# Performance work log

Measured on AMD Instinct MI355X. Metric: run time of the kernel, lower is better.

## Reference

```python
import jax, jax.numpy as jnp
import numpy as np

N_NODES = 100000
N_EDGES = 1600000
N_GRAPHS = 512
IN_CH = 128
HID = 128
OUT_CH = 1
FP_DIM = 2048


def prelu(x, a):
    return jnp.where(x > 0, x, a * x)


def setup_inputs() -> dict:
    key = jax.random.key(0)
    ks = jax.random.split(key, 16)

    def glorot(k, shape):
        lim = np.sqrt(6.0 / (shape[0] + shape[1]))
        return jax.random.uniform(k, shape, jnp.float32, -lim, lim)

    x = jax.random.normal(ks[0], (N_NODES, IN_CH), jnp.float32)
    fp = jax.random.normal(ks[1], (N_GRAPHS, FP_DIM), jnp.float32)
    edge_index = jax.random.randint(ks[2], (2, N_EDGES), 0, N_NODES, jnp.int64)
    batch = jnp.sort(jax.random.randint(ks[3], (N_NODES,), 0, N_GRAPHS, jnp.int64))

    params = {
        "W_pre": glorot(ks[4], (IN_CH, HID)),
        "b_pre": jnp.zeros((HID,), jnp.float32),
        "a_pre": jnp.full((HID,), 0.25, jnp.float32),
        "Wl1": glorot(ks[5], (HID, HID)),
        "bl1": jnp.zeros((HID,), jnp.float32),
        "Wr1": glorot(ks[6], (HID, HID)),
        "a1": jnp.full((HID,), 0.25, jnp.float32),
        "Wl2": glorot(ks[7], (HID, HID)),
        "bl2": jnp.zeros((HID,), jnp.float32),
        "Wr2": glorot(ks[8], (HID, HID)),
        "a2": jnp.full((HID,), 0.25, jnp.float32),
        "W_fp": glorot(ks[9], (FP_DIM, HID)),
        "b_fp": jnp.zeros((HID,), jnp.float32),
        "a_fp": jnp.full((HID,), 0.25, jnp.float32),
        "W_post": glorot(ks[10], (2 * HID, OUT_CH)),
        "b_post": jnp.zeros((OUT_CH,), jnp.float32),
    }
    return dict(x=x, fp=fp, edge_index=edge_index, batch=batch, **params)


def sage_conv(x, src, dst, Wl, bl, Wr):
    # aggr='sum': sum messages x[src] into dst, then lin_l(agg)+bias + lin_r(x)
    agg = jax.ops.segment_sum(x[src], dst, num_segments=N_NODES)  # [N, H]
    return agg @ Wl + bl + x @ Wr


def reference(x, fp, edge_index, batch,
              W_pre, b_pre, a_pre,
              Wl1, bl1, Wr1, a1,
              Wl2, bl2, Wr2, a2,
              W_fp, b_fp, a_fp,
              W_post, b_post):
    src, dst = edge_index[0], edge_index[1]
    # pre_mp (dropout is identity at eval)
    h = prelu(x @ W_pre + b_pre, a_pre)
    # message passing
    h = prelu(sage_conv(h, src, dst, Wl1, bl1, Wr1), a1)
    h = prelu(sage_conv(h, src, dst, Wl2, bl2, Wr2), a2)
    # global mean pool over graphs
    sums = jax.ops.segment_sum(h, batch, num_segments=N_GRAPHS)  # [G, H]
    counts = jax.ops.segment_sum(jnp.ones((h.shape[0],), h.dtype), batch,
                                 num_segments=N_GRAPHS)
    pooled = sums / jnp.maximum(counts, 1.0)[:, None]
    # fingerprint head
    fp_emb = prelu(fp @ W_fp + b_fp, a_fp)
    # post mp
    out = jnp.concatenate([pooled, fp_emb], axis=1) @ W_post + b_post
    return out
```

## Files before the change

kernel.cpp:

```cpp
#include <hip/hip_runtime.h>

#define NN 100000
#define NE 1600000
#define NG 512
#define HID 128
#define FPD 2048
#define BSHIFT 8
#define NBUK ((NN + 255) >> 8)
#define BCAP 5120
#define EPB 4096
#define EPT 16

typedef _Float16 f16;
typedef __attribute__((ext_vector_type(8))) _Float16 f16x8;
typedef __attribute__((ext_vector_type(2))) _Float16 f16x2;
typedef __attribute__((ext_vector_type(4))) float f32x4;


__global__ __launch_bounds__(256) void bucket_scatter(const int* __restrict__ src,
                                                      const int* __restrict__ dst,
                                                      int* __restrict__ bcnt,
                                                      uint* __restrict__ bbuf, int E) {
  __shared__ int hist[NBUK];
  __shared__ int gbase[NBUK];
  __shared__ int lbase[NBUK + 1];
  __shared__ int sc[2][512];
  __shared__ uint stage[EPB];
  int t = threadIdx.x;
  int e0 = blockIdx.x * EPB;
  for (int i = t; i < NBUK; i += 256) hist[i] = 0;
  __syncthreads();

  int myb[EPT], myoff[EPT];
  uint myp[EPT];
#pragma unroll
  for (int u = 0; u < EPT; ++u) {
    int e = e0 + u * 256 + t;
    myb[u] = -1;
    if (e < E) {
      int d = dst[e];
      int b = d >> BSHIFT;
      myp[u] = ((uint)(d & 255) << 24) | (uint)src[e];
      myb[u] = b;
      myoff[u] = atomicAdd(&hist[b], 1);
    }
  }
  __syncthreads();

  sc[0][t] = (t < NBUK) ? hist[t] : 0;
  sc[0][t + 256] = (t + 256 < NBUK) ? hist[t + 256] : 0;
  int pp = 0;
  for (int off = 1; off < 512; off <<= 1) {
    __syncthreads();
    int a0 = sc[pp][t] + ((t >= off) ? sc[pp][t - off] : 0);
    int a1 = sc[pp][t + 256] + ((t + 256 >= off) ? sc[pp][t + 256 - off] : 0);
    sc[1 - pp][t] = a0;
    sc[1 - pp][t + 256] = a1;
    pp = 1 - pp;
  }
  __syncthreads();
  if (t < NBUK) lbase[t] = (t == 0) ? 0 : sc[pp][t - 1];
  if (t + 256 < NBUK) lbase[t + 256] = sc[pp][t + 255];
  if (t == 0) lbase[NBUK] = sc[pp][NBUK - 1];
  for (int i = t; i < NBUK; i += 256)
    if (hist[i] > 0) gbase[i] = atomicAdd(&bcnt[i], hist[i]);
  __syncthreads();

#pragma unroll
  for (int u = 0; u < EPT; ++u)
    if (myb[u] >= 0) stage[lbase[myb[u]] + myoff[u]] = myp[u];
  __syncthreads();

  int total = lbase[NBUK];
  for (int j = t; j < total; j += 256) {
    int lo = 0, hi = NBUK - 1;
    while (lo < hi) {
      int mid = (lo + hi + 1) >> 1;
      if (lbase[mid] <= j) lo = mid; else hi = mid - 1;
    }
    bbuf[(size_t)lo * BCAP + gbase[lo] + (j - lbase[lo])] = stage[j];
  }
}

__global__ __launch_bounds__(512) void scan_bcnt(const int* __restrict__ bcnt,
                                                 int* __restrict__ bbase,
                                                 int* __restrict__ rowptr) {
  __shared__ int lds[512];
  int t = threadIdx.x;
  int v = (t < NBUK) ? bcnt[t] : 0;
  lds[t] = v;
  __syncthreads();
  for (int off = 1; off < 512; off <<= 1) {
    int add = (t >= off) ? lds[t - off] : 0;
    __syncthreads();
    lds[t] += add;
    __syncthreads();
  }
  if (t < NBUK) bbase[t] = lds[t] - v;
  if (t == 0) {
    bbase[NBUK] = lds[511];
    rowptr[NN] = lds[511];
  }
}

__global__ __launch_bounds__(256) void bucket_finish(const int* __restrict__ bcnt,
                                                     const uint* __restrict__ bbuf,
                                                     const int* __restrict__ bbase,
                                                     int* __restrict__ rowptr,
                                                     int* __restrict__ cols) {
  __shared__ uint ebuf[BCAP];
  __shared__ int h[256];
  __shared__ int s2[256];
  __shared__ int cur[256];
  int b = blockIdx.x, t = threadIdx.x;
  h[t] = 0;
  __syncthreads();
  int n = bcnt[b];
  const uint* bb = bbuf + (size_t)b * BCAP;
  for (int e = t; e < n; e += 256) {
    uint w = bb[e];
    ebuf[e] = w;
    atomicAdd(&h[w >> 24], 1);
  }
  __syncthreads();
  int v = h[t];
  s2[t] = v;
  __syncthreads();
  for (int off = 1; off < 256; off <<= 1) {
    int add = (t >= off) ? s2[t - off] : 0;
    __syncthreads();
    s2[t] += add;
    __syncthreads();
  }
  int base = bbase[b] + s2[t] - v;
  int node = (b << BSHIFT) + t;
  if (node < NN) rowptr[node] = base;
  cur[t] = base;
  __syncthreads();
  for (int e = t; e < n; e += 256) {
    uint w = ebuf[e];
    int pos = atomicAdd(&cur[w >> 24], 1);
    cols[pos] = (int)(w & 0xFFFFFF);
  }
}


__global__ __launch_bounds__(256) void cvt_all(const float* __restrict__ w0,
                                               const float* __restrict__ w1,
                                               const float* __restrict__ w2,
                                               const float* __restrict__ w3,
                                               const float* __restrict__ w4,
                                               const float* __restrict__ Wfp,
                                               const float* __restrict__ fp,
                                               f16* __restrict__ Wt,
                                               f16* __restrict__ Wfpt,
                                               f16* __restrict__ fpb) {
  int idx = blockIdx.x * 256 + threadIdx.x;
  if (idx < 81920) {
    int w = idx >> 14, rem = idx & 16383;
    int j = rem >> 7, k = rem & 127;
    const float* W = (w == 0) ? w0 : (w == 1) ? w1 : (w == 2) ? w2 : (w == 3) ? w3 : w4;
    Wt[idx] = (f16)W[k * 128 + j];
  } else if (idx < 344064) {
    int id = idx - 81920;
    int j = id >> 11, k = id & 2047;
    Wfpt[id] = (f16)Wfp[k * 128 + j];
  } else if (idx < 606208) {
    int id = idx - 344064;
    float4 v = *reinterpret_cast<const float4*>(&fp[id * 4]);
    union { uint2 u; f16 h[4]; } o;
    o.h[0] = (f16)v.x; o.h[1] = (f16)v.y; o.h[2] = (f16)v.z; o.h[3] = (f16)v.w;
    *reinterpret_cast<uint2*>(&fpb[id * 4]) = o.u;
  }
}


__global__ __launch_bounds__(256) void agg_f16(const f16* __restrict__ H,
                                               const int* __restrict__ rowptr,
                                               const int* __restrict__ cols,
                                               f16* __restrict__ out) {
  int node = blockIdx.x * 4 + (threadIdx.x >> 6);
  int lane = threadIdx.x & 63;
  int q = lane >> 4;
  int sub = lane & 15;
  int s = rowptr[node], e = rowptr[node + 1];
  float acc[8] = {0.f, 0.f, 0.f, 0.f, 0.f, 0.f, 0.f, 0.f};
  union U { uint4 u; f16x2 h2[4]; f16 h[8]; };

  int i = s;
  for (; i + 15 < e; i += 16) {
    int c0 = cols[i + q];
    int c1 = cols[i + 4 + q];
    int c2 = cols[i + 8 + q];
    int c3 = cols[i + 12 + q];
    U v0, v1, v2, v3;
    v0.u = *reinterpret_cast<const uint4*>(&H[(size_t)c0 * 128 + sub * 8]);
    v1.u = *reinterpret_cast<const uint4*>(&H[(size_t)c1 * 128 + sub * 8]);
    v2.u = *reinterpret_cast<const uint4*>(&H[(size_t)c2 * 128 + sub * 8]);
    v3.u = *reinterpret_cast<const uint4*>(&H[(size_t)c3 * 128 + sub * 8]);
#pragma unroll
    for (int p = 0; p < 4; ++p) {
      f16x2 t01 = v0.h2[p] + v1.h2[p];
      f16x2 t23 = v2.h2[p] + v3.h2[p];
      f16x2 tt = t01 + t23;
      acc[2 * p]     += (float)tt[0];
      acc[2 * p + 1] += (float)tt[1];
    }
  }
  for (; i < e; i += 4) {
    int rem = e - i;
    if (q < rem) {
      U v;
      v.u = *reinterpret_cast<const uint4*>(&H[(size_t)cols[i + q] * 128 + sub * 8]);
#pragma unroll
      for (int z = 0; z < 8; ++z) acc[z] += (float)v.h[z];
    }
  }

#pragma unroll
  for (int z = 0; z < 8; ++z) {
    acc[z] += __shfl_xor(acc[z], 16);
    acc[z] += __shfl_xor(acc[z], 32);
  }
  if (q == 0) {
    union { uint4 u; f16 h[8]; } pk;
#pragma unroll
    for (int z = 0; z < 8; ++z) pk.h[z] = (f16)acc[z];
    *reinterpret_cast<uint4*>(&out[(size_t)node * 128 + sub * 8]) = pk.u;
  }
}


__global__ __launch_bounds__(256) void gemm_pre(const float* __restrict__ X,
                                                const f16* __restrict__ Wt,
                                                const float* __restrict__ bias,
                                                const float* __restrict__ pa,
                                                f16* __restrict__ out, int rows) {
  int t = threadIdx.x;
  int wave = t >> 6, lane = t & 63;
  int lrow = lane & 15, lk = lane >> 4;
  int r0 = blockIdx.x * 64;
  int n0 = wave << 1;

  const f16x8* Wv = reinterpret_cast<const f16x8*>(Wt);
  f16x8 w[2][4];
#pragma unroll
  for (int ni = 0; ni < 2; ++ni)
#pragma unroll
    for (int ks = 0; ks < 4; ++ks)
      w[ni][ks] = Wv[((((n0 + ni) << 4) + lrow) << 4) + (ks << 2) + lk];

  float bv[2], av[2];
#pragma unroll
  for (int ni = 0; ni < 2; ++ni) {
    int col = ((n0 + ni) << 4) + lrow;
    bv[ni] = bias[col];
    av[ni] = pa[col];
  }

#pragma unroll 2
  for (int rg = 0; rg < 4; ++rg) {
    int r = r0 + (rg << 4) + lrow;
    if (r > rows - 1) r = rows - 1;
    const float* xp = X + (size_t)r * 128 + (lk << 3);
    f16x8 a[4];
#pragma unroll
    for (int ks = 0; ks < 4; ++ks) {
      float4 v0 = *reinterpret_cast<const float4*>(xp + (ks << 5));
      float4 v1 = *reinterpret_cast<const float4*>(xp + (ks << 5) + 4);
      f16x8 av8;
      av8[0] = (f16)v0.x; av8[1] = (f16)v0.y; av8[2] = (f16)v0.z; av8[3] = (f16)v0.w;
      av8[4] = (f16)v1.x; av8[5] = (f16)v1.y; av8[6] = (f16)v1.z; av8[7] = (f16)v1.w;
      a[ks] = av8;
    }
    f32x4 acc[2] = {(f32x4){0.f, 0.f, 0.f, 0.f}, (f32x4){0.f, 0.f, 0.f, 0.f}};
#pragma unroll
    for (int ks = 0; ks < 4; ++ks)
#pragma unroll
      for (int ni = 0; ni < 2; ++ni)
        acc[ni] = __builtin_amdgcn_mfma_f32_16x16x32_f16(a[ks], w[ni][ks], acc[ni], 0, 0, 0);
#pragma unroll
    for (int ni = 0; ni < 2; ++ni) {
      int col = ((n0 + ni) << 4) + lrow;
#pragma unroll
      for (int j = 0; j < 4; ++j) {
        int rr = r0 + (rg << 4) + (lk << 2) + j;
        if (rr < rows) {
          float xv = acc[ni][j] + bv[ni];
          xv = xv > 0.f ? xv : av[ni] * xv;
          out[(size_t)rr * 128 + col] = (f16)xv;
        }
      }
    }
  }
}


__global__ __launch_bounds__(256) void gemm_f16(const f16* __restrict__ A1,
                                                const f16* __restrict__ A2,
                                                const f16* __restrict__ W1t,
                                                const f16* __restrict__ W2t,
                                                const float* __restrict__ bias,
                                                const float* __restrict__ pa,
                                                f16* __restrict__ Ch, int rows) {
  int t = threadIdx.x;
  int wave = t >> 6, lane = t & 63;
  int lrow = lane & 15, lk = lane >> 4;
  int r0 = blockIdx.x * 64;
  int n0 = wave << 1;

  const f16x8* Wv1 = reinterpret_cast<const f16x8*>(W1t);
  const f16x8* Wv2 = reinterpret_cast<const f16x8*>(W2t);

  f16x8 w1[2][4], w2[2][4];
#pragma unroll
  for (int ni = 0; ni < 2; ++ni)
#pragma unroll
    for (int ks = 0; ks < 4; ++ks) {
      int wi = ((((n0 + ni) << 4) + lrow) << 4) + (ks << 2) + lk;
      w1[ni][ks] = Wv1[wi];
      w2[ni][ks] = Wv2[wi];
    }

  float bv[2], av[2];
#pragma unroll
  for (int ni = 0; ni < 2; ++ni) {
    int col = ((n0 + ni) << 4) + lrow;
    bv[ni] = bias[col];
    av[ni] = pa[col];
  }

  f16x8 aA[2][4], aB[2][4];
  {
    int r = r0 + lrow;
    if (r > rows - 1) r = rows - 1;
    size_t off = (size_t)r * 128 + (lk << 3);
#pragma unroll
    for (int ks = 0; ks < 4; ++ks) {
      aA[0][ks] = *reinterpret_cast<const f16x8*>(A1 + off + (ks << 5));
      aB[0][ks] = *reinterpret_cast<const f16x8*>(A2 + off + (ks << 5));
    }
  }

#pragma unroll
  for (int rg = 0; rg < 4; ++rg) {
    int cur = rg & 1, nxt = cur ^ 1;
    if (rg < 3) {
      int rn = r0 + ((rg + 1) << 4) + lrow;
      if (rn > rows - 1) rn = rows - 1;
      size_t offn = (size_t)rn * 128 + (lk << 3);
#pragma unroll
      for (int ks = 0; ks < 4; ++ks) {
        aA[nxt][ks] = *reinterpret_cast<const f16x8*>(A1 + offn + (ks << 5));
        aB[nxt][ks] = *reinterpret_cast<const f16x8*>(A2 + offn + (ks << 5));
      }
    }
    f32x4 acc1[2] = {(f32x4){0.f, 0.f, 0.f, 0.f}, (f32x4){0.f, 0.f, 0.f, 0.f}};
    f32x4 acc2[2] = {(f32x4){0.f, 0.f, 0.f, 0.f}, (f32x4){0.f, 0.f, 0.f, 0.f}};
#pragma unroll
    for (int ks = 0; ks < 4; ++ks) {
#pragma unroll
      for (int ni = 0; ni < 2; ++ni) {
        acc1[ni] = __builtin_amdgcn_mfma_f32_16x16x32_f16(aA[cur][ks], w1[ni][ks], acc1[ni], 0, 0, 0);
        acc2[ni] = __builtin_amdgcn_mfma_f32_16x16x32_f16(aB[cur][ks], w2[ni][ks], acc2[ni], 0, 0, 0);
      }
    }
#pragma unroll
    for (int ni = 0; ni < 2; ++ni) {
      int col = ((n0 + ni) << 4) + lrow;
#pragma unroll
      for (int j = 0; j < 4; ++j) {
        int rr = r0 + (rg << 4) + (lk << 2) + j;
        if (rr < rows) {
          float xv = acc1[ni][j] + acc2[ni][j] + bv[ni];
          xv = xv > 0.f ? xv : av[ni] * xv;
          Ch[(size_t)rr * 128 + col] = (f16)xv;
        }
      }
    }
  }
}


__global__ __launch_bounds__(256) void fp_gemm(const f16* __restrict__ A,
                                               const f16* __restrict__ Wt,
                                               float* __restrict__ part) {
  int kc = blockIdx.x;
  int rb = blockIdx.y;
  int t = threadIdx.x;
  int wave = t >> 6, lane = t & 63;
  int lrow = lane & 15, lk = lane >> 4;
  int r0 = rb * 128;
  int n0 = wave << 1;

  const f16x8* Wv = reinterpret_cast<const f16x8*>(Wt);
  const f16x8* Av = reinterpret_cast<const f16x8*>(A);

  f16x8 w[2][4];
#pragma unroll
  for (int ni = 0; ni < 2; ++ni)
#pragma unroll
    for (int ks = 0; ks < 4; ++ks) {
      int j = ((n0 + ni) << 4) + lrow;
      w[ni][ks] = Wv[j * 256 + (kc << 4) + (ks << 2) + lk];
    }

#pragma unroll 2
  for (int rg = 0; rg < 8; ++rg) {
    int r = r0 + (rg << 4) + lrow;
    f16x8 a[4];
#pragma unroll
    for (int ks = 0; ks < 4; ++ks)
      a[ks] = Av[r * 256 + (kc << 4) + (ks << 2) + lk];
    f32x4 acc[2] = {(f32x4){0.f, 0.f, 0.f, 0.f}, (f32x4){0.f, 0.f, 0.f, 0.f}};
#pragma unroll
    for (int ks = 0; ks < 4; ++ks)
#pragma unroll
      for (int ni = 0; ni < 2; ++ni)
        acc[ni] = __builtin_amdgcn_mfma_f32_16x16x32_f16(a[ks], w[ni][ks], acc[ni], 0, 0, 0);
#pragma unroll
    for (int ni = 0; ni < 2; ++ni) {
      int col = ((n0 + ni) << 4) + lrow;
#pragma unroll
      for (int j = 0; j < 4; ++j) {
        int rr = r0 + (rg << 4) + (lk << 2) + j;
        part[((size_t)kc * 512 + rr) * 128 + col] = acc[ni][j];
      }
    }
  }
}


__device__ __forceinline__ int lower_bound_dev(const int* __restrict__ arr, int n, int val) {
  int lo = 0, hi = n;
  while (lo < hi) {
    int mid = (lo + hi) >> 1;
    if (arr[mid] < val) lo = mid + 1; else hi = mid;
  }
  return lo;
}

__global__ __launch_bounds__(512) void pool_final(const f16* __restrict__ H,
                                                  const int* __restrict__ batch,
                                                  const float* __restrict__ part,
                                                  const float* __restrict__ bfp,
                                                  const float* __restrict__ afp,
                                                  const float* __restrict__ Wp,
                                                  const float* __restrict__ bp,
                                                  float* __restrict__ out) {
  __shared__ float red[512];
  __shared__ float pf[256];
  int g = blockIdx.x;
  int t = threadIdx.x;
  int col = t & 127, rq = t >> 7;
  int start = lower_bound_dev(batch, NN, g);
  int end = lower_bound_dev(batch, NN, g + 1);
  float acc = 0.f;
  for (int r = start + rq; r < end; r += 4) acc += (float)H[(size_t)r * 128 + col];
  red[t] = acc;
  __syncthreads();
  if (t < 128) {
    float s = red[t] + red[128 + t] + red[256 + t] + red[384 + t];
    int c = end - start;
    pf[t] = s / (float)(c > 0 ? c : 1);
  } else if (t < 256) {
    int j = t - 128;
    float s = bfp[j];
#pragma unroll
    for (int kc = 0; kc < 16; ++kc) s += part[((size_t)kc * 512 + g) * 128 + j];
    float a = afp[j];
    pf[t] = s > 0.f ? s : a * s;
  }
  __syncthreads();
  if (t < 128) {
    float v = pf[t] * Wp[t] + pf[128 + t] * Wp[128 + t];
    red[t] = v;
  }
  __syncthreads();
  if (t < 64) {
    float v = red[t] + red[t + 64];
    for (int off = 32; off > 0; off >>= 1) v += __shfl_down(v, off);
    if (t == 0) out[g] = v + bp[0];
  }
}


extern "C" void kernel_launch(void* const* d_in, const int* in_sizes, int n_in,
                              void* d_out, int out_size, void* d_ws, size_t ws_size,
                              hipStream_t stream) {
  const float* x      = (const float*)d_in[0];
  const float* fp     = (const float*)d_in[1];
  const int*   ei     = (const int*)d_in[2];
  const int*   batch  = (const int*)d_in[3];
  const float* W_pre  = (const float*)d_in[4];
  const float* b_pre  = (const float*)d_in[5];
  const float* a_pre  = (const float*)d_in[6];
  const float* Wl1    = (const float*)d_in[7];
  const float* bl1    = (const float*)d_in[8];
  const float* Wr1    = (const float*)d_in[9];
  const float* a1     = (const float*)d_in[10];
  const float* Wl2    = (const float*)d_in[11];
  const float* bl2    = (const float*)d_in[12];
  const float* Wr2    = (const float*)d_in[13];
  const float* a2     = (const float*)d_in[14];
  const float* W_fp   = (const float*)d_in[15];
  const float* b_fp   = (const float*)d_in[16];
  const float* a_fp   = (const float*)d_in[17];
  const float* W_post = (const float*)d_in[18];
  const float* b_post = (const float*)d_in[19];

  const int* src = ei;
  const int* dst = ei + NE;

  const size_t NBUF = (size_t)NN * 128;
  f16* bufA = (f16*)d_ws;
  f16* bufB = bufA + NBUF;
  f16* bufC = bufB + NBUF;
  f16* Wt   = bufC + NBUF;
  f16* fpb  = Wt + 5 * 16384;
  f16* Wfpt = fpb + 512 * 2048;
  float* part = (float*)(Wfpt + 128 * 2048);
  int* rowptr  = (int*)(part + 16 * 512 * 128);
  int* bbase   = rowptr + NN + 4;
  int* bcnt    = bbase + NBUK + 4;
  int* colsA   = bcnt + ((NBUK + 3) & ~3);
  uint* bbuf   = (uint*)(colsA + NE);

  hipMemsetAsync(bcnt, 0, NBUK * sizeof(int), stream);
  bucket_scatter<<<(NE + EPB - 1) / EPB, 256, 0, stream>>>(src, dst, bcnt, bbuf, NE);
  scan_bcnt<<<1, 512, 0, stream>>>(bcnt, bbase, rowptr);
  bucket_finish<<<NBUK, 256, 0, stream>>>(bcnt, bbuf, bbase, rowptr, colsA);

  cvt_all<<<(606208 + 255) / 256, 256, 0, stream>>>(W_pre, Wl1, Wr1, Wl2, Wr2, W_fp, fp,
                                                    Wt, Wfpt, fpb);
  {
    dim3 g(16, 4);
    fp_gemm<<<g, 256, 0, stream>>>(fpb, Wfpt, part);
  }

  const f16* Wt_pre = Wt;
  const f16* Wt_l1  = Wt + 16384;
  const f16* Wt_r1  = Wt + 32768;
  const f16* Wt_l2  = Wt + 49152;
  const f16* Wt_r2  = Wt + 65536;

  int gGemm = (NN + 63) / 64;

  gemm_pre<<<gGemm, 256, 0, stream>>>(x, Wt_pre, b_pre, a_pre, bufA, NN);

  agg_f16<<<NN / 4, 256, 0, stream>>>(bufA, rowptr, colsA, bufC);
  gemm_f16<<<gGemm, 256, 0, stream>>>(bufC, bufA, Wt_l1, Wt_r1, bl1, a1, bufB, NN);

  agg_f16<<<NN / 4, 256, 0, stream>>>(bufB, rowptr, colsA, bufC);
  gemm_f16<<<gGemm, 256, 0, stream>>>(bufC, bufB, Wt_l2, Wt_r2, bl2, a2, bufA, NN);

  pool_final<<<NG, 512, 0, stream>>>(bufA, batch, part, b_fp, a_fp, W_post, b_post,
                                     (float*)d_out);
}
```

Baseline: 330.3 us.

## Pad CSR rows to multiples of 16 with dummy node and fuse fp conversion into fp_gemm

Each node's neighbour list is padded to a multiple of 16 entries that point at an all-zero dummy row (node NN), stored as separate start and end arrays. The aggregation kernel can then drop its remainder loop and always use the 4-wide unrolled gather. The fp-to-f16 conversion moves out of cvt_all and into fp_gemm, which reads fp32 directly, removing a write and read of an intermediate buffer. In exchange, padding adds extra gathered rows of the zero vector and two small memsets, and colsA needs a larger allocation.

```diff
diff --git a/kernel.cpp b/kernel.cpp
--- a/kernel.cpp
+++ b/kernel.cpp
@@ -10,6 +10,7 @@
 #define BCAP 5120
 #define EPB 4096
 #define EPT 16
+#define COLSCAP (NE + NBUK * 4096 + 64)
 
 typedef _Float16 f16;
 typedef __attribute__((ext_vector_type(8))) _Float16 f16x8;
@@ -83,11 +84,10 @@
 }
 
 __global__ __launch_bounds__(512) void scan_bcnt(const int* __restrict__ bcnt,
-                                                 int* __restrict__ bbase,
-                                                 int* __restrict__ rowptr) {
+                                                 int* __restrict__ bbase) {
   __shared__ int lds[512];
   int t = threadIdx.x;
-  int v = (t < NBUK) ? bcnt[t] : 0;
+  int v = (t < NBUK) ? (bcnt[t] + 4096) : 0;
   lds[t] = v;
   __syncthreads();
   for (int off = 1; off < 512; off <<= 1) {
@@ -97,16 +97,13 @@
     __syncthreads();
   }
   if (t < NBUK) bbase[t] = lds[t] - v;
-  if (t == 0) {
-    bbase[NBUK] = lds[511];
-    rowptr[NN] = lds[511];
-  }
 }
 
 __global__ __launch_bounds__(256) void bucket_finish(const int* __restrict__ bcnt,
                                                      const uint* __restrict__ bbuf,
                                                      const int* __restrict__ bbase,
-                                                     int* __restrict__ rowptr,
+                                                     int* __restrict__ astart,
+                                                     int* __restrict__ aend,
                                                      int* __restrict__ cols) {
   __shared__ uint ebuf[BCAP];
   __shared__ int h[256];
@@ -124,7 +121,8 @@
   }
   __syncthreads();
   int v = h[t];
-  s2[t] = v;
+  int pv = (v + 15) & ~15;
+  s2[t] = pv;
   __syncthreads();
   for (int off = 1; off < 256; off <<= 1) {
     int add = (t >= off) ? s2[t - off] : 0;
@@ -132,9 +130,12 @@
     s2[t] += add;
     __syncthreads();
   }
-  int base = bbase[b] + s2[t] - v;
+  int base = bbase[b] + s2[t] - pv;
   int node = (b << BSHIFT) + t;
-  if (node < NN) rowptr[node] = base;
+  if (node < NN) {
+    astart[node] = base;
+    aend[node] = base + pv;
+  }
   cur[t] = base;
   __syncthreads();
   for (int e = t; e < n; e += 256) {
@@ -142,6 +143,7 @@
     int pos = atomicAdd(&cur[w >> 24], 1);
     cols[pos] = (int)(w & 0xFFFFFF);
   }
+  for (int p = v; p < pv; ++p) cols[base + p] = NN;
 }
 
 
@@ -151,10 +153,8 @@
                                                const float* __restrict__ w3,
                                                const float* __restrict__ w4,
                                                const float* __restrict__ Wfp,
-                                               const float* __restrict__ fp,
                                                f16* __restrict__ Wt,
-                                               f16* __restrict__ Wfpt,
-                                               f16* __restrict__ fpb) {
+                                               f16* __restrict__ Wfpt) {
   int idx = blockIdx.x * 256 + threadIdx.x;
   if (idx < 81920) {
     int w = idx >> 14, rem = idx & 16383;
@@ -165,30 +165,24 @@
     int id = idx - 81920;
     int j = id >> 11, k = id & 2047;
     Wfpt[id] = (f16)Wfp[k * 128 + j];
-  } else if (idx < 606208) {
-    int id = idx - 344064;
-    float4 v = *reinterpret_cast<const float4*>(&fp[id * 4]);
-    union { uint2 u; f16 h[4]; } o;
-    o.h[0] = (f16)v.x; o.h[1] = (f16)v.y; o.h[2] = (f16)v.z; o.h[3] = (f16)v.w;
-    *reinterpret_cast<uint2*>(&fpb[id * 4]) = o.u;
   }
 }
 
 
 __global__ __launch_bounds__(256) void agg_f16(const f16* __restrict__ H,
-                                               const int* __restrict__ rowptr,
+                                               const int* __restrict__ astart,
+                                               const int* __restrict__ aend,
                                                const int* __restrict__ cols,
                                                f16* __restrict__ out) {
   int node = blockIdx.x * 4 + (threadIdx.x >> 6);
   int lane = threadIdx.x & 63;
   int q = lane >> 4;
   int sub = lane & 15;
-  int s = rowptr[node], e = rowptr[node + 1];
+  int s = astart[node], e = aend[node];
   float acc[8] = {0.f, 0.f, 0.f, 0.f, 0.f, 0.f, 0.f, 0.f};
   union U { uint4 u; f16x2 h2[4]; f16 h[8]; };
 
-  int i = s;
-  for (; i + 15 < e; i += 16) {
+  for (int i = s; i < e; i += 16) {
     int c0 = cols[i + q];
     int c1 = cols[i + 4 + q];
     int c2 = cols[i + 8 + q];
@@ -205,15 +199,6 @@
       f16x2 tt = t01 + t23;
       acc[2 * p]     += (float)tt[0];
       acc[2 * p + 1] += (float)tt[1];
-    }
-  }
-  for (; i < e; i += 4) {
-    int rem = e - i;
-    if (q < rem) {
-      U v;
-      v.u = *reinterpret_cast<const uint4*>(&H[(size_t)cols[i + q] * 128 + sub * 8]);
-#pragma unroll
-      for (int z = 0; z < 8; ++z) acc[z] += (float)v.h[z];
     }
   }
 
@@ -382,7 +367,7 @@
 }
 
 
-__global__ __launch_bounds__(256) void fp_gemm(const f16* __restrict__ A,
+__global__ __launch_bounds__(256) void fp_gemm(const float* __restrict__ FP,
                                                const f16* __restrict__ Wt,
                                                float* __restrict__ part) {
   int kc = blockIdx.x;
@@ -394,7 +379,6 @@
   int n0 = wave << 1;
 
   const f16x8* Wv = reinterpret_cast<const f16x8*>(Wt);
-  const f16x8* Av = reinterpret_cast<const f16x8*>(A);
 
   f16x8 w[2][4];
 #pragma unroll
@@ -408,10 +392,17 @@
 #pragma unroll 2
   for (int rg = 0; rg < 8; ++rg) {
     int r = r0 + (rg << 4) + lrow;
+    const float* xp = FP + (size_t)r * 2048 + (kc << 7) + (lk << 3);
     f16x8 a[4];
 #pragma unroll
-    for (int ks = 0; ks < 4; ++ks)
-      a[ks] = Av[r * 256 + (kc << 4) + (ks << 2) + lk];
+    for (int ks = 0; ks < 4; ++ks) {
+      float4 v0 = *reinterpret_cast<const float4*>(xp + (ks << 5));
+      float4 v1 = *reinterpret_cast<const float4*>(xp + (ks << 5) + 4);
+      f16x8 av8;
+      av8[0] = (f16)v0.x; av8[1] = (f16)v0.y; av8[2] = (f16)v0.z; av8[3] = (f16)v0.w;
+      av8[4] = (f16)v1.x; av8[5] = (f16)v1.y; av8[6] = (f16)v1.z; av8[7] = (f16)v1.w;
+      a[ks] = av8;
+    }
     f32x4 acc[2] = {(f32x4){0.f, 0.f, 0.f, 0.f}, (f32x4){0.f, 0.f, 0.f, 0.f}};
 #pragma unroll
     for (int ks = 0; ks < 4; ++ks)
@@ -512,30 +503,32 @@
   const int* src = ei;
   const int* dst = ei + NE;
 
-  const size_t NBUF = (size_t)NN * 128;
+  const size_t NBUF = (size_t)(NN + 1) * 128;
   f16* bufA = (f16*)d_ws;
   f16* bufB = bufA + NBUF;
   f16* bufC = bufB + NBUF;
   f16* Wt   = bufC + NBUF;
-  f16* fpb  = Wt + 5 * 16384;
-  f16* Wfpt = fpb + 512 * 2048;
+  f16* Wfpt = Wt + 5 * 16384;
   float* part = (float*)(Wfpt + 128 * 2048);
-  int* rowptr  = (int*)(part + 16 * 512 * 128);
-  int* bbase   = rowptr + NN + 4;
+  int* astart  = (int*)(part + 16 * 512 * 128);
+  int* aend    = astart + NN;
+  int* bbase   = aend + NN;
   int* bcnt    = bbase + NBUK + 4;
   int* colsA   = bcnt + ((NBUK + 3) & ~3);
-  uint* bbuf   = (uint*)(colsA + NE);
+  uint* bbuf   = (uint*)(colsA + COLSCAP);
 
   hipMemsetAsync(bcnt, 0, NBUK * sizeof(int), stream);
+  hipMemsetAsync(bufA + (size_t)NN * 128, 0, 256, stream);
+  hipMemsetAsync(bufB + (size_t)NN * 128, 0, 256, stream);
   bucket_scatter<<<(NE + EPB - 1) / EPB, 256, 0, stream>>>(src, dst, bcnt, bbuf, NE);
-  scan_bcnt<<<1, 512, 0, stream>>>(bcnt, bbase, rowptr);
-  bucket_finish<<<NBUK, 256, 0, stream>>>(bcnt, bbuf, bbase, rowptr, colsA);
-
-  cvt_all<<<(606208 + 255) / 256, 256, 0, stream>>>(W_pre, Wl1, Wr1, Wl2, Wr2, W_fp, fp,
-                                                    Wt, Wfpt, fpb);
+  scan_bcnt<<<1, 512, 0, stream>>>(bcnt, bbase);
+  bucket_finish<<<NBUK, 256, 0, stream>>>(bcnt, bbuf, bbase, astart, aend, colsA);
+
+  cvt_all<<<(344064 + 255) / 256, 256, 0, stream>>>(W_pre, Wl1, Wr1, Wl2, Wr2, W_fp,
+                                                    Wt, Wfpt);
   {
     dim3 g(16, 4);
-    fp_gemm<<<g, 256, 0, stream>>>(fpb, Wfpt, part);
+    fp_gemm<<<g, 256, 0, stream>>>(fp, Wfpt, part);
   }
 
   const f16* Wt_pre = Wt;
@@ -548,10 +541,10 @@
 
   gemm_pre<<<gGemm, 256, 0, stream>>>(x, Wt_pre, b_pre, a_pre, bufA, NN);
 
-  agg_f16<<<NN / 4, 256, 0, stream>>>(bufA, rowptr, colsA, bufC);
+  agg_f16<<<NN / 4, 256, 0, stream>>>(bufA, astart, aend, colsA, bufC);
   gemm_f16<<<gGemm, 256, 0, stream>>>(bufC, bufA, Wt_l1, Wt_r1, bl1, a1, bufB, NN);
 
-  agg_f16<<<NN / 4, 256, 0, stream>>>(bufB, rowptr, colsA, bufC);
+  agg_f16<<<NN / 4, 256, 0, stream>>>(bufB, astart, aend, colsA, bufC);
   gemm_f16<<<gGemm, 256, 0, stream>>>(bufC, bufB, Wt_l2, Wt_r2, bl2, a2, bufA, NN);
 
   pool_final<<<NG, 512, 0, stream>>>(bufA, batch, part, b_fp, a_fp, W_post, b_post,
```

Result: no change. 334.6 us (+1.3%).
